# Kernel tuning notes

Hardware: AMD Instinct MI355X
Metric: run time of the kernel (lower is better)

Reference implementation:

```python
import jax, jax.numpy as jnp
import numpy as np

B = 128          # batch_size
S = 8192         # max_seq_length
V = 128000       # vocab size (token_count rows)


def setup_inputs() -> dict:
    key = jax.random.key(0)
    k1, k2, k3 = jax.random.split(key, 3)
    return {
        "tokens": jax.random.randint(k1, (B,), 0, V, dtype=jnp.int32),
        "last_token_index": jax.random.randint(k2, (B, 1), 0, S - 1, dtype=jnp.int32),
        "attention_mask": jnp.zeros((B, S, 1), jnp.float32),
        "generated_tokens": jnp.zeros((B, S, 1), jnp.int32),
        "generated_tokens_streaming": jnp.zeros((B, S, 1), jnp.int32),
        "generated_index": jax.random.randint(k3, (B, 1), 0, S - 1, dtype=jnp.int32),
        "token_count": jnp.zeros((B, V, 1), jnp.int32),
    }


def reference(tokens, last_token_index, attention_mask, generated_tokens,
              generated_tokens_streaming, generated_index, token_count):
    # Single-step token-gen postprocess (forward_token_gen_length_eq_one).
    b = jnp.arange(B)

    # 1. advance and clamp last_token_index
    lti = jnp.minimum(last_token_index + 1, S - 1)               # (B,1)

    # 2. set attention_mask[b, lti, 0] = 1 (batched scatter of ones)
    attention_mask = attention_mask.at[b, lti[:, 0], 0].set(
        jnp.ones((B,), attention_mask.dtype))

    # 3. write new tokens at generated_index (both regular and streaming buffers)
    generated_tokens = generated_tokens.at[b, generated_index[:, 0], 0].set(tokens)
    generated_tokens_streaming = generated_tokens_streaming.at[
        b, generated_index[:, 0], 0].set(tokens)

    # 4. advance and clamp generated_index
    gi = jnp.minimum(generated_index + 1, S - 1)                 # (B,1)

    # 5. per-batch histogram increment: token_count[b, tokens[b], 0] += 1
    token_count = token_count.at[b, tokens, 0].add(
        jnp.ones((B,), token_count.dtype))

    return (tokens, lti, attention_mask, generated_tokens,
            generated_tokens_streaming, gi, token_count)
```

## Files before the change

kernel.cpp:

```cpp
#include <hip/hip_runtime.h>

#define BB 128
#define SS 8192
#define VV 128000

#define OFF_TOK 0
#define OFF_LTI (OFF_TOK + BB)
#define OFF_MASK (OFF_LTI + BB)
#define OFF_GEN (OFF_MASK + BB * SS)
#define OFF_STR (OFF_GEN + BB * SS)
#define OFF_GI  (OFF_STR + BB * SS)
#define OFF_CNT (OFF_GI + BB)

typedef float f32x4 __attribute__((ext_vector_type(4)));
typedef int   i32x4 __attribute__((ext_vector_type(4)));

#define NB_S   256
#define NB_CNT 4000
#define NB_TOTAL (3 * NB_S + NB_CNT + 1)

__global__ void __launch_bounds__(256)
k_fused(const int* __restrict__ tokens,
        const int* __restrict__ lti_in,
        const float* __restrict__ mask_in,
        const int* __restrict__ gen_in,
        const int* __restrict__ str_in,
        const int* __restrict__ gi_in,
        const int* __restrict__ cnt_in,
        float* __restrict__ out)
{
    const int bid = blockIdx.x;
    const int tid = threadIdx.x;

    if (bid < 3 * NB_S) {
        const int region = bid >> 8;
        const int rbid   = bid & 255;
        #pragma unroll
        for (int j = 0; j < 4; ++j) {
            const int    c  = rbid * 1024 + j * 256 + tid;
            const int    b  = c >> 11;
            const int    s0 = (c & 2047) << 2;
            const size_t e  = (size_t)c << 2;

            if (region == 0) {
                f32x4 m = __builtin_nontemporal_load((const f32x4*)(mask_in + e));
                const int lti_new = min(lti_in[b] + 1, SS - 1);
                if ((unsigned)(lti_new - s0) < 4u)
                    m[lti_new - s0] = 1.0f;
                __builtin_nontemporal_store(m, (f32x4*)(out + OFF_MASK + e));
            } else {
                const int* src = (region == 1) ? gen_in : str_in;
                const int  dst = (region == 1) ? OFF_GEN : OFF_STR;
                i32x4 g = __builtin_nontemporal_load((const i32x4*)(src + e));
                f32x4 go;
                go[0] = (float)g[0]; go[1] = (float)g[1];
                go[2] = (float)g[2]; go[3] = (float)g[3];
                const int gi_old = gi_in[b];
                if ((unsigned)(gi_old - s0) < 4u)
                    go[gi_old - s0] = (float)tokens[b];
                __builtin_nontemporal_store(go, (f32x4*)(out + dst + e));
            }
        }
    } else if (bid < 3 * NB_S + NB_CNT) {
        const int rbid = bid - 3 * NB_S;
        #pragma unroll
        for (int j = 0; j < 4; ++j) {
            const int    c  = rbid * 1024 + j * 256 + tid;
            const int    b  = c / 32000;
            const int    v0 = (c - b * 32000) << 2;
            const size_t e  = (size_t)c << 2;

            i32x4 cc = __builtin_nontemporal_load((const i32x4*)(cnt_in + e));
            f32x4 co;
            co[0] = (float)cc[0]; co[1] = (float)cc[1];
            co[2] = (float)cc[2]; co[3] = (float)cc[3];
            const int tok = tokens[b];
            if ((unsigned)(tok - v0) < 4u)
                co[tok - v0] += 1.0f;
            __builtin_nontemporal_store(co, (f32x4*)(out + OFF_CNT + e));
        }
    } else {
        if (tid < BB) {
            out[OFF_TOK + tid] = (float)tokens[tid];
            out[OFF_LTI + tid] = (float)min(lti_in[tid] + 1, SS - 1);
            out[OFF_GI  + tid] = (float)min(gi_in[tid] + 1, SS - 1);
        }
    }
}

extern "C" void kernel_launch(void* const* d_in, const int* in_sizes, int n_in,
                              void* d_out, int out_size, void* d_ws, size_t ws_size,
                              hipStream_t stream) {
    const int*   tokens = (const int*)  d_in[0];
    const int*   lti    = (const int*)  d_in[1];
    const float* mask   = (const float*)d_in[2];
    const int*   gen    = (const int*)  d_in[3];
    const int*   strm   = (const int*)  d_in[4];
    const int*   gi     = (const int*)  d_in[5];
    const int*   cnt    = (const int*)  d_in[6];
    float* out = (float*)d_out;

    k_fused<<<dim3(NB_TOTAL), dim3(256), 0, stream>>>(
        tokens, lti, mask, gen, strm, gi, cnt, out);
}
```

Measured before the change: 144.4 us.

## Switch to grid-stride persistent blocks and use regular stores for outputs

Replaces the fixed per-region block mapping (4769 blocks, 4 chunks each) with a 2048-block grid where each block strides over up to 10 chunk-blocks across a unified index space covering mask, generated, streaming and count regions. Output stores change from nontemporal to ordinary stores, which may let writes go through cache differently. The goal is to cut block launch/tail overhead and improve coalescing per iteration; the cost is more loop control and per-element region branching.

```diff
diff --git a/kernel.cpp b/kernel.cpp
--- a/kernel.cpp
+++ b/kernel.cpp
@@ -15,9 +15,10 @@
 typedef float f32x4 __attribute__((ext_vector_type(4)));
 typedef int   i32x4 __attribute__((ext_vector_type(4)));
 
-#define NB_S   256
-#define NB_CNT 4000
-#define NB_TOTAL (3 * NB_S + NB_CNT + 1)
+#define CHUNKS_S_PER 262144
+#define CHUNKS_S_ALL 786432
+#define CB_TOTAL     19072
+#define GRID         2048
 
 __global__ void __launch_bounds__(256)
 k_fused(const int* __restrict__ tokens,
@@ -32,58 +33,51 @@
     const int bid = blockIdx.x;
     const int tid = threadIdx.x;
 
-    if (bid < 3 * NB_S) {
-        const int region = bid >> 8;
-        const int rbid   = bid & 255;
-        #pragma unroll
-        for (int j = 0; j < 4; ++j) {
-            const int    c  = rbid * 1024 + j * 256 + tid;
-            const int    b  = c >> 11;
-            const int    s0 = (c & 2047) << 2;
-            const size_t e  = (size_t)c << 2;
+    if (bid == 0 && tid < BB) {
+        out[OFF_TOK + tid] = (float)tokens[tid];
+        out[OFF_LTI + tid] = (float)min(lti_in[tid] + 1, SS - 1);
+        out[OFF_GI  + tid] = (float)min(gi_in[tid] + 1, SS - 1);
+    }
 
+    #pragma unroll
+    for (int k = 0; k < 10; ++k) {
+        const int cb = k * GRID + bid;
+        if (cb >= CB_TOTAL) break;
+        const int c = cb * 256 + tid;
+
+        if (c < CHUNKS_S_ALL) {
+            const int    region = c >> 18;
+            const int    cr     = c & (CHUNKS_S_PER - 1);
+            const int    b      = cr >> 11;
+            const int    s0     = (cr & 2047) << 2;
+            const size_t e      = (size_t)cr << 2;
             if (region == 0) {
                 f32x4 m = __builtin_nontemporal_load((const f32x4*)(mask_in + e));
                 const int lti_new = min(lti_in[b] + 1, SS - 1);
                 if ((unsigned)(lti_new - s0) < 4u)
                     m[lti_new - s0] = 1.0f;
-                __builtin_nontemporal_store(m, (f32x4*)(out + OFF_MASK + e));
+                *(f32x4*)(out + OFF_MASK + e) = m;
             } else {
-                const int* src = (region == 1) ? gen_in : str_in;
-                const int  dst = (region == 1) ? OFF_GEN : OFF_STR;
+                const int* src  = (region == 1) ? gen_in : str_in;
+                float*     dstp = out + ((region == 1) ? OFF_GEN : OFF_STR);
                 i32x4 g = __builtin_nontemporal_load((const i32x4*)(src + e));
-                f32x4 go;
-                go[0] = (float)g[0]; go[1] = (float)g[1];
-                go[2] = (float)g[2]; go[3] = (float)g[3];
+                f32x4 go = { (float)g[0], (float)g[1], (float)g[2], (float)g[3] };
                 const int gi_old = gi_in[b];
                 if ((unsigned)(gi_old - s0) < 4u)
                     go[gi_old - s0] = (float)tokens[b];
-                __builtin_nontemporal_store(go, (f32x4*)(out + dst + e));
+                *(f32x4*)(dstp + e) = go;
             }
-        }
-    } else if (bid < 3 * NB_S + NB_CNT) {
-        const int rbid = bid - 3 * NB_S;
-        #pragma unroll
-        for (int j = 0; j < 4; ++j) {
-            const int    c  = rbid * 1024 + j * 256 + tid;
-            const int    b  = c / 32000;
-            const int    v0 = (c - b * 32000) << 2;
-            const size_t e  = (size_t)c << 2;
-
+        } else {
+            const int    cr = c - CHUNKS_S_ALL;
+            const int    b  = cr / 32000;
+            const int    v0 = (cr - b * 32000) << 2;
+            const size_t e  = (size_t)cr << 2;
             i32x4 cc = __builtin_nontemporal_load((const i32x4*)(cnt_in + e));
-            f32x4 co;
-            co[0] = (float)cc[0]; co[1] = (float)cc[1];
-            co[2] = (float)cc[2]; co[3] = (float)cc[3];
+            f32x4 co = { (float)cc[0], (float)cc[1], (float)cc[2], (float)cc[3] };
             const int tok = tokens[b];
             if ((unsigned)(tok - v0) < 4u)
                 co[tok - v0] += 1.0f;
-            __builtin_nontemporal_store(co, (f32x4*)(out + OFF_CNT + e));
-        }
-    } else {
-        if (tid < BB) {
-            out[OFF_TOK + tid] = (float)tokens[tid];
-            out[OFF_LTI + tid] = (float)min(lti_in[tid] + 1, SS - 1);
-            out[OFF_GI  + tid] = (float)min(gi_in[tid] + 1, SS - 1);
+            *(f32x4*)(out + OFF_CNT + e) = co;
         }
     }
 }
@@ -100,6 +94,6 @@
     const int*   cnt    = (const int*)  d_in[6];
     float* out = (float*)d_out;
 
-    k_fused<<<dim3(NB_TOTAL), dim3(256), 0, stream>>>(
+    k_fused<<<dim3(GRID), dim3(256), 0, stream>>>(
         tokens, lti, mask, gen, strm, gi, cnt, out);
 }
```

After: 140.6 us. 2.7% less time.
